# Optimization experiments

Measured on AMD Instinct MI355X. Metric: run time of the kernel, lower is better.

## Reference

```python
import jax, jax.numpy as jnp
import numpy as np

NUM_QUBITS = 512
NUM_CORES = 16
CORE_SIZE = 64
HIDDEN = 128
BATCH = 2048


def setup_inputs() -> dict:
    key = jax.random.key(0)
    k1, k2, k3 = jax.random.split(key, 3)
    last_assignment = jax.random.randint(k1, (BATCH, NUM_QUBITS), 0, NUM_CORES, dtype=jnp.int32)
    adjacency = jnp.ones((NUM_CORES, NUM_CORES), dtype=jnp.float32)  # all-to-all core graph
    qubit_embedding = jax.random.normal(k2, (NUM_QUBITS + 1, HIDDEN), dtype=jnp.float32)
    gcn_weight = jax.random.normal(k3, (HIDDEN, HIDDEN), dtype=jnp.float32) * (1.0 / np.sqrt(HIDDEN))
    gcn_bias = jnp.zeros((HIDDEN,), dtype=jnp.float32)
    return {
        'last_assignment': last_assignment,
        'adjacency': adjacency,
        'qubit_embedding': qubit_embedding,
        'gcn_weight': gcn_weight,
        'gcn_bias': gcn_bias,
    }


def reference(last_assignment, adjacency, qubit_embedding, gcn_weight, gcn_bias):
    B, Q = last_assignment.shape
    C = adjacency.shape[0]
    # --- replace the sequential per-qubit scatter loop with a single cumsum ---
    # pos[b,q] = number of earlier qubits assigned to the same core (the loop's
    # running counter idx); core index C (the extra row) always writes slot 0
    # because the loop resets its counter every iteration.
    oh = jax.nn.one_hot(last_assignment, C + 1, dtype=jnp.int32)        # [B,Q,C+1]
    cnt = jnp.cumsum(oh, axis=1)                                        # inclusive counts
    pos = jnp.take_along_axis(cnt, last_assignment[..., None], axis=2)[..., 0] - 1
    pos = jnp.where(last_assignment == C, 0, pos)
    buf = jnp.full((B, C + 1, CORE_SIZE), Q, dtype=jnp.int32)           # padding id = num_qubits
    b_idx = jnp.arange(B)[:, None]
    q_idx = jnp.broadcast_to(jnp.arange(Q, dtype=jnp.int32)[None, :], (B, Q))
    buf = buf.at[b_idx, last_assignment, pos].set(q_idx, mode='drop')
    buf = buf[:, :C, :]                                                 # drop overflow core row
    # --- embedding (padding row forced to zero, as nn.Embedding padding_idx) ---
    tbl = qubit_embedding.at[Q].set(0.0)
    qubit_embs = tbl[buf]                                               # [B,C,core_size,H]
    core_embs = qubit_embs.max(axis=2)                                  # [B,C,H]
    # --- GCNConv(add_self_loops=False): D^{-1/2} A D^{-1/2} (X W^T) + b ---
    deg = adjacency.sum(axis=0)
    dinv = jnp.where(deg > 0, 1.0 / jnp.sqrt(deg), 0.0)
    a_norm = adjacency * dinv[:, None] * dinv[None, :]                  # symmetric norm
    h = jnp.einsum('bch,oh->bco', core_embs, gcn_weight)                # lin (PyG: x @ W^T)
    out = jnp.einsum('ij,bjo->bio', a_norm, h) + gcn_bias               # [B,C,H]
    return out
```

## Files before the change

kernel.cpp:

```cpp
#include <hip/hip_runtime.h>
#include <stdint.h>

typedef unsigned short u16;
typedef unsigned int u32;
typedef unsigned long long u64;

typedef __bf16 bf16x8 __attribute__((ext_vector_type(8)));
typedef float f32x4 __attribute__((ext_vector_type(4)));
typedef u16 u16x8 __attribute__((ext_vector_type(8)));

#define NQ 512
#define NC 16
#define NH 128
#define NB 2048
#define ESTRIDE 136
#define HSTRIDE 24
#define QE_KEYS (513*128)
#define WT_OFF  QE_KEYS
#define GW_ELEMS (128*128)

static __device__ __forceinline__ u16 f2bf_rne(float f){
  u32 u = __float_as_uint(f);
  u += 0x7fffu + ((u>>16)&1u);
  return (u16)(u>>16);
}
static __device__ __forceinline__ u32 pack_rne(float lo, float hi){
  return (u32)f2bf_rne(lo) | ((u32)f2bf_rne(hi)<<16);
}
static __device__ __forceinline__ u16 key_of(float f){
  u16 b = f2bf_rne(f);
  return (b & 0x8000u) ? (u16)~b : (u16)(b | 0x8000u);
}
static __device__ __forceinline__ u16 unkey(u16 k){
  return (k & 0x8000u) ? (u16)(k ^ 0x8000u) : (u16)~k;
}

union Frag { u32 u[4]; uint4 u4; bf16x8 f; };
union U8   { u16x8 v; int w[4]; uint4 u4; u16 h[8]; };

__global__ void prepass_kernel(const float* __restrict__ qe,
                               const float* __restrict__ gw,
                               u16* __restrict__ ws)
{
  int idx = blockIdx.x * 256 + threadIdx.x;
  if (idx < QE_KEYS/8) {
    int i8 = idx * 8;
    uint4 o;
    if (i8 >= 512*NH) {
      o.x = 0x80008000u; o.y = 0x80008000u; o.z = 0x80008000u; o.w = 0x80008000u;
    } else {
      const float4* p = (const float4*)(qe + i8);
      float4 a = p[0], b = p[1];
      o.x = (u32)key_of(a.x) | ((u32)key_of(a.y)<<16);
      o.y = (u32)key_of(a.z) | ((u32)key_of(a.w)<<16);
      o.z = (u32)key_of(b.x) | ((u32)key_of(b.y)<<16);
      o.w = (u32)key_of(b.z) | ((u32)key_of(b.w)<<16);
    }
    *(uint4*)(ws + i8) = o;
  } else if (idx < QE_KEYS/8 + GW_ELEMS/8) {
    int j8 = (idx - QE_KEYS/8) * 8;
    const float4* p = (const float4*)(gw + j8);
    float4 a = p[0], b = p[1];
    uint4 o;
    o.x = pack_rne(a.x, a.y); o.y = pack_rne(a.z, a.w);
    o.z = pack_rne(b.x, b.y); o.w = pack_rne(b.z, b.w);
    *(uint4*)(ws + WT_OFF + j8) = o;
  }
}

static __device__ __forceinline__ void wave_reduce_max(U8& A){
  U8 B;
  #pragma unroll
  for (int j = 0; j < 4; ++j) B.w[j] = __shfl_xor(A.w[j], 16);
  A.v = __builtin_elementwise_max(A.v, B.v);
  #pragma unroll
  for (int j = 0; j < 4; ++j) B.w[j] = __shfl_xor(A.w[j], 32);
  A.v = __builtin_elementwise_max(A.v, B.v);
}

__global__ __launch_bounds__(256, 4)
void core_snapshot_kernel(const int* __restrict__ la,
                          const float* __restrict__ adj,
                          const u16* __restrict__ ws,
                          const float* __restrict__ gb,
                          float* __restrict__ outp)
{
  __shared__ __align__(16) u16 sE[16*ESTRIDE];
  __shared__ __align__(16) u16 sHB[128*HSTRIDE];
  __shared__ __align__(16) u16 sList[16*64];
  __shared__ u32 sHist[8*16];
  __shared__ u32 sBase[8*16];
  __shared__ u32 sCnt[16];
  __shared__ float sDinv[16];

  const int tid  = threadIdx.x;
  const int lane = tid & 63;
  const int wv   = tid >> 6;
  const int m    = lane & 15;
  const int quad = lane >> 4;
  const int b    = blockIdx.x;
  const u16* qt  = ws;
  const u16* wt  = ws + WT_OFF;

  ((uint2*)sList)[tid] = make_uint2(0x02000200u, 0x02000200u);

  int av[2]; u32 intra[2];
  const u64 lmask = (1ull << lane) - 1ull;
  #pragma unroll
  for (int r = 0; r < 2; ++r) {
    int ch = wv*2 + r;
    av[r] = la[b*NQ + ch*64 + lane];
  }
  #pragma unroll
  for (int r = 0; r < 2; ++r) {
    int ch = wv*2 + r;
    #pragma unroll
    for (int c = 0; c < 16; ++c) {
      u64 mk = __ballot(av[r] == c);
      if (lane == c)  sHist[ch*16 + c] = (u32)__popcll(mk);
      if (av[r] == c) intra[r] = (u32)__popcll(mk & lmask);
    }
  }
  if (tid < 16) {
    float s = 0.f;
    for (int i = 0; i < 16; ++i) s += adj[i*16 + tid];
    sDinv[tid] = (s > 0.f) ? (1.0f / sqrtf(s)) : 0.f;
  }
  __syncthreads();
  if (tid < 16) {
    u32 run = 0;
    #pragma unroll
    for (int ch = 0; ch < 8; ++ch) { sBase[ch*16 + tid] = run; run += sHist[ch*16 + tid]; }
    sCnt[tid] = run;
  }
  __syncthreads();
  #pragma unroll
  for (int r = 0; r < 2; ++r) {
    int ch = wv*2 + r;
    u32 rank = sBase[ch*16 + av[r]] + intra[r];
    if (rank < 64) sList[av[r]*64 + (rank&3)*16 + (rank>>2)] = (u16)(ch*64 + lane);
  }
  __syncthreads();

  {
    const u16* qb = qt + m*8;
    #pragma unroll
    for (int half = 0; half < 2; ++half) {
      const int ca = wv*4 + half*2, cb = ca + 1;
      U8 Sa0, Sa1, Sb0, Sb1;
      Sa0.u4 = *(const uint4*)&sList[ca*64 + quad*16];
      Sa1.u4 = *(const uint4*)&sList[ca*64 + quad*16 + 8];
      Sb0.u4 = *(const uint4*)&sList[cb*64 + quad*16];
      Sb1.u4 = *(const uint4*)&sList[cb*64 + quad*16 + 8];
      const int cna = (int)sCnt[ca], cnb = (int)sCnt[cb];
      U8 A, B; A.v = (u16x8)0; B.v = (u16x8)0;
      {
        U8 Ta[4], Tb[4];
        #pragma unroll
        for (int k = 0; k < 4; ++k) {
          Ta[k].u4 = *(const uint4*)(qb + (int)Sa0.h[k]*NH);
          Tb[k].u4 = *(const uint4*)(qb + (int)Sb0.h[k]*NH);
        }
        #pragma unroll
        for (int k = 0; k < 4; ++k) {
          A.v = __builtin_elementwise_max(A.v, Ta[k].v);
          B.v = __builtin_elementwise_max(B.v, Tb[k].v);
        }
        #pragma unroll
        for (int k = 0; k < 4; ++k) {
          Ta[k].u4 = *(const uint4*)(qb + (int)Sa0.h[k+4]*NH);
          Tb[k].u4 = *(const uint4*)(qb + (int)Sb0.h[k+4]*NH);
        }
        #pragma unroll
        for (int k = 0; k < 4; ++k) {
          A.v = __builtin_elementwise_max(A.v, Ta[k].v);
          B.v = __builtin_elementwise_max(B.v, Tb[k].v);
        }
      }
      if (cna > 32) {
        U8 Ta[8];
        #pragma unroll
        for (int k = 0; k < 8; ++k) Ta[k].u4 = *(const uint4*)(qb + (int)Sa1.h[k]*NH);
        #pragma unroll
        for (int k = 0; k < 8; ++k) A.v = __builtin_elementwise_max(A.v, Ta[k].v);
      }
      if (cnb > 32) {
        U8 Tb[8];
        #pragma unroll
        for (int k = 0; k < 8; ++k) Tb[k].u4 = *(const uint4*)(qb + (int)Sb1.h[k]*NH);
        #pragma unroll
        for (int k = 0; k < 8; ++k) B.v = __builtin_elementwise_max(B.v, Tb[k].v);
      }
      wave_reduce_max(A);
      wave_reduce_max(B);
      U8 Z; Z.v = (u16x8)(u16)0x8000u;
      if (cna < 64) A.v = __builtin_elementwise_max(A.v, Z.v);
      if (cnb < 64) B.v = __builtin_elementwise_max(B.v, Z.v);
      if (quad == 0) {
        uint4 e;
        e.x = (u32)unkey(A.h[0]) | ((u32)unkey(A.h[1])<<16);
        e.y = (u32)unkey(A.h[2]) | ((u32)unkey(A.h[3])<<16);
        e.z = (u32)unkey(A.h[4]) | ((u32)unkey(A.h[5])<<16);
        e.w = (u32)unkey(A.h[6]) | ((u32)unkey(A.h[7])<<16);
        *(uint4*)&sE[ca*ESTRIDE + m*8] = e;
        e.x = (u32)unkey(B.h[0]) | ((u32)unkey(B.h[1])<<16);
        e.y = (u32)unkey(B.h[2]) | ((u32)unkey(B.h[3])<<16);
        e.z = (u32)unkey(B.h[4]) | ((u32)unkey(B.h[5])<<16);
        e.w = (u32)unkey(B.h[6]) | ((u32)unkey(B.h[7])<<16);
        *(uint4*)&sE[cb*ESTRIDE + m*8] = e;
      }
    }
  }
  __syncthreads();

  {
    bf16x8 af[4];
    #pragma unroll
    for (int ks = 0; ks < 4; ++ks)
      af[ks] = *(const bf16x8*)&sE[m*ESTRIDE + ks*32 + quad*8];
    #pragma unroll
    for (int t = 0; t < 2; ++t) {
      int o = (wv*2 + t)*16 + m;
      f32x4 acc = {0.f, 0.f, 0.f, 0.f};
      #pragma unroll
      for (int ks = 0; ks < 4; ++ks) {
        bf16x8 bfr = *(const bf16x8*)(wt + o*NH + ks*32 + quad*8);
        acc = __builtin_amdgcn_mfma_f32_16x16x32_bf16(af[ks], bfr, acc, 0, 0, 0);
      }
      *(u32*)&sHB[o*HSTRIDE + quad*4]     = pack_rne(acc[0], acc[1]);
      *(u32*)&sHB[o*HSTRIDE + quad*4 + 2] = pack_rne(acc[2], acc[3]);
    }
  }
  __syncthreads();

  Frag afr2;
  #pragma unroll
  for (int jj = 0; jj < 4; ++jj) {
    float lo = 0.f, hi = 0.f;
    if (quad < 2) {
      int k0 = quad*8 + jj*2;
      lo = adj[m*16 + k0]     * sDinv[m] * sDinv[k0];
      hi = adj[m*16 + k0 + 1] * sDinv[m] * sDinv[k0 + 1];
    }
    afr2.u[jj] = pack_rne(lo, hi);
  }
  #pragma unroll
  for (int t = 0; t < 2; ++t) {
    int o = (wv*2 + t)*16 + m;
    float biasv = gb[(wv*2 + t)*16 + m];
    Frag bfr;
    if (quad < 2) bfr.u4 = *(const uint4*)&sHB[o*HSTRIDE + quad*8];
    else { bfr.u[0]=0; bfr.u[1]=0; bfr.u[2]=0; bfr.u[3]=0; }
    f32x4 acc = {biasv, biasv, biasv, biasv};
    acc = __builtin_amdgcn_mfma_f32_16x16x32_bf16(afr2.f, bfr.f, acc, 0, 0, 0);
    float* op = outp + b*(NC*NH) + o;
    #pragma unroll
    for (int r = 0; r < 4; ++r) op[(quad*4 + r)*NH] = acc[r];
  }
}

extern "C" void kernel_launch(void* const* d_in, const int* in_sizes, int n_in,
                              void* d_out, int out_size, void* d_ws, size_t ws_size,
                              hipStream_t stream) {
  const int*   la  = (const int*)d_in[0];
  const float* adj = (const float*)d_in[1];
  const float* qe  = (const float*)d_in[2];
  const float* gw  = (const float*)d_in[3];
  const float* gb  = (const float*)d_in[4];
  float* outp = (float*)d_out;
  u16* ws = (u16*)d_ws;

  int pre_threads = QE_KEYS/8 + GW_ELEMS/8;
  prepass_kernel<<<(pre_threads + 255)/256, 256, 0, stream>>>(qe, gw, ws);
  core_snapshot_kernel<<<NB, 256, 0, stream>>>(la, adj, ws, gb, outp);
}
```

Before: 94.70 us.

## Stage embedding table in LDS and process eight batch items per block

The bf16 key table (513x128, about 140KB with padding) is copied into shared memory once per 1024-thread block. Each block then handles 8 batch items, two at a time with two 8-wave teams, so the gathers read LDS instead of global/L2. The launch drops from 2048 blocks to 256. The large LDS footprint allows only one block per CU, and the per-block table load plus the extra barriers in each pair loop could offset the gain.

```diff
diff --git a/kernel.cpp b/kernel.cpp
--- a/kernel.cpp
+++ b/kernel.cpp
@@ -13,8 +13,11 @@
 #define NC 16
 #define NH 128
 #define NB 2048
+#define IPB 8
+#define NBLK (NB/IPB)
+#define TSTRIDE 136
 #define ESTRIDE 136
-#define HSTRIDE 24
+#define HSTRIDE 16
 #define QE_KEYS (513*128)
 #define WT_OFF  QE_KEYS
 #define GW_ELEMS (128*128)
@@ -78,47 +81,41 @@
   A.v = __builtin_elementwise_max(A.v, B.v);
 }
 
-__global__ __launch_bounds__(256, 4)
+__global__ __launch_bounds__(1024, 4)
 void core_snapshot_kernel(const int* __restrict__ la,
                           const float* __restrict__ adj,
                           const u16* __restrict__ ws,
                           const float* __restrict__ gb,
                           float* __restrict__ outp)
 {
-  __shared__ __align__(16) u16 sE[16*ESTRIDE];
-  __shared__ __align__(16) u16 sHB[128*HSTRIDE];
-  __shared__ __align__(16) u16 sList[16*64];
-  __shared__ u32 sHist[8*16];
-  __shared__ u32 sBase[8*16];
-  __shared__ u32 sCnt[16];
+  __shared__ __align__(16) u16 sTab[513*TSTRIDE];
+  __shared__ __align__(16) u16 sList[2][16*64];
+  __shared__ __align__(16) u16 sE[2][16*ESTRIDE];
+  __shared__ __align__(16) u16 sHB[2][128*HSTRIDE];
+  __shared__ u32 sHist[2][8*16];
+  __shared__ u32 sBase[2][8*16];
+  __shared__ u32 sCnt[2][16];
   __shared__ float sDinv[16];
 
   const int tid  = threadIdx.x;
   const int lane = tid & 63;
   const int wv   = tid >> 6;
+  const int team = wv >> 3;
+  const int wt8  = wv & 7;
   const int m    = lane & 15;
   const int quad = lane >> 4;
-  const int b    = blockIdx.x;
-  const u16* qt  = ws;
   const u16* wt  = ws + WT_OFF;
 
-  ((uint2*)sList)[tid] = make_uint2(0x02000200u, 0x02000200u);
-
-  int av[2]; u32 intra[2];
-  const u64 lmask = (1ull << lane) - 1ull;
-  #pragma unroll
-  for (int r = 0; r < 2; ++r) {
-    int ch = wv*2 + r;
-    av[r] = la[b*NQ + ch*64 + lane];
-  }
-  #pragma unroll
-  for (int r = 0; r < 2; ++r) {
-    int ch = wv*2 + r;
+  {
+    const uint4* src = (const uint4*)ws;
     #pragma unroll
-    for (int c = 0; c < 16; ++c) {
-      u64 mk = __ballot(av[r] == c);
-      if (lane == c)  sHist[ch*16 + c] = (u32)__popcll(mk);
-      if (av[r] == c) intra[r] = (u32)__popcll(mk & lmask);
+    for (int i = 0; i < 9; ++i) {
+      int idx = tid + i*1024;
+      if (idx < QE_KEYS/8) {
+        uint4 v = src[idx];
+        int row = idx >> 4, col8 = (idx & 15) << 3;
+        *(uint4*)&sTab[row*TSTRIDE + col8] = v;
+      }
     }
   }
   if (tid < 16) {
@@ -127,39 +124,67 @@
     sDinv[tid] = (s > 0.f) ? (1.0f / sqrtf(s)) : 0.f;
   }
   __syncthreads();
-  if (tid < 16) {
-    u32 run = 0;
+
+  Frag afr2;
+  #pragma unroll
+  for (int jj = 0; jj < 4; ++jj) {
+    float lo = 0.f, hi = 0.f;
+    if (quad < 2) {
+      int k0 = quad*8 + jj*2;
+      lo = adj[m*16 + k0]     * sDinv[m] * sDinv[k0];
+      hi = adj[m*16 + k0 + 1] * sDinv[m] * sDinv[k0 + 1];
+    }
+    afr2.u[jj] = pack_rne(lo, hi);
+  }
+  const int ocol = wt8*16 + m;
+  const float biasv = gb[ocol];
+  const u64 lmask = (1ull << lane) - 1ull;
+
+  for (int pair = 0; pair < IPB/2; ++pair) {
+    const int item = blockIdx.x*IPB + pair*2 + team;
+
+    if (tid < 256)
+      ((uint4*)sList)[tid] = make_uint4(0x02000200u,0x02000200u,0x02000200u,0x02000200u);
+
+    const int avv = la[item*NQ + wt8*64 + lane];
+    u32 intra = 0;
     #pragma unroll
-    for (int ch = 0; ch < 8; ++ch) { sBase[ch*16 + tid] = run; run += sHist[ch*16 + tid]; }
-    sCnt[tid] = run;
-  }
-  __syncthreads();
-  #pragma unroll
-  for (int r = 0; r < 2; ++r) {
-    int ch = wv*2 + r;
-    u32 rank = sBase[ch*16 + av[r]] + intra[r];
-    if (rank < 64) sList[av[r]*64 + (rank&3)*16 + (rank>>2)] = (u16)(ch*64 + lane);
-  }
-  __syncthreads();
-
-  {
-    const u16* qb = qt + m*8;
-    #pragma unroll
-    for (int half = 0; half < 2; ++half) {
-      const int ca = wv*4 + half*2, cb = ca + 1;
+    for (int c = 0; c < 16; ++c) {
+      u64 mk = __ballot(avv == c);
+      if (lane == c) sHist[team][wt8*16 + c] = (u32)__popcll(mk);
+      if (avv == c)  intra = (u32)__popcll(mk & lmask);
+    }
+    __syncthreads();
+    if (tid < 32) {
+      int t = tid >> 4, c = tid & 15;
+      u32 run = 0;
+      #pragma unroll
+      for (int ch = 0; ch < 8; ++ch) { sBase[t][ch*16 + c] = run; run += sHist[t][ch*16 + c]; }
+      sCnt[t][c] = run;
+    }
+    __syncthreads();
+    {
+      u32 rank = sBase[team][wt8*16 + avv] + intra;
+      if (rank < 64) sList[team][avv*64 + (rank&3)*16 + (rank>>2)] = (u16)(wt8*64 + lane);
+    }
+    __syncthreads();
+
+    {
+      const int ca = wt8*2, cb = ca + 1;
       U8 Sa0, Sa1, Sb0, Sb1;
-      Sa0.u4 = *(const uint4*)&sList[ca*64 + quad*16];
-      Sa1.u4 = *(const uint4*)&sList[ca*64 + quad*16 + 8];
-      Sb0.u4 = *(const uint4*)&sList[cb*64 + quad*16];
-      Sb1.u4 = *(const uint4*)&sList[cb*64 + quad*16 + 8];
-      const int cna = (int)sCnt[ca], cnb = (int)sCnt[cb];
+      Sa0.u4 = *(const uint4*)&sList[team][ca*64 + quad*16];
+      Sa1.u4 = *(const uint4*)&sList[team][ca*64 + quad*16 + 8];
+      Sb0.u4 = *(const uint4*)&sList[team][cb*64 + quad*16];
+      Sb1.u4 = *(const uint4*)&sList[team][cb*64 + quad*16 + 8];
+      const int cna = (int)sCnt[team][ca], cnb = (int)sCnt[team][cb];
       U8 A, B; A.v = (u16x8)0; B.v = (u16x8)0;
+      const u16* tb = sTab + m*8;
       {
         U8 Ta[4], Tb[4];
         #pragma unroll
         for (int k = 0; k < 4; ++k) {
-          Ta[k].u4 = *(const uint4*)(qb + (int)Sa0.h[k]*NH);
-          Tb[k].u4 = *(const uint4*)(qb + (int)Sb0.h[k]*NH);
+          Ta[k].u4 = *(const uint4*)(tb + (int)Sa0.h[k]*TSTRIDE);
+          Tb[k].u4 = *(const uint4*)(tb + (int)Sb0.h[k]*TSTRIDE);
         }
         #pragma unroll
         for (int k = 0; k < 4; ++k) {
@@ -168,8 +193,8 @@
         }
         #pragma unroll
         for (int k = 0; k < 4; ++k) {
-          Ta[k].u4 = *(const uint4*)(qb + (int)Sa0.h[k+4]*NH);
-          Tb[k].u4 = *(const uint4*)(qb + (int)Sb0.h[k+4]*NH);
+          Ta[k].u4 = *(const uint4*)(tb + (int)Sa0.h[k+4]*TSTRIDE);
+          Tb[k].u4 = *(const uint4*)(tb + (int)Sb0.h[k+4]*TSTRIDE);
         }
         #pragma unroll
         for (int k = 0; k < 4; ++k) {
@@ -180,14 +205,14 @@
       if (cna > 32) {
         U8 Ta[8];
         #pragma unroll
-        for (int k = 0; k < 8; ++k) Ta[k].u4 = *(const uint4*)(qb + (int)Sa1.h[k]*NH);
+        for (int k = 0; k < 8; ++k) Ta[k].u4 = *(const uint4*)(tb + (int)Sa1.h[k]*TSTRIDE);
         #pragma unroll
         for (int k = 0; k < 8; ++k) A.v = __builtin_elementwise_max(A.v, Ta[k].v);
       }
       if (cnb > 32) {
         U8 Tb[8];
         #pragma unroll
-        for (int k = 0; k < 8; ++k) Tb[k].u4 = *(const uint4*)(qb + (int)Sb1.h[k]*NH);
+        for (int k = 0; k < 8; ++k) Tb[k].u4 = *(const uint4*)(tb + (int)Sb1.h[k]*TSTRIDE);
         #pragma unroll
         for (int k = 0; k < 8; ++k) B.v = __builtin_elementwise_max(B.v, Tb[k].v);
       }
@@ -202,60 +227,43 @@
         e.y = (u32)unkey(A.h[2]) | ((u32)unkey(A.h[3])<<16);
         e.z = (u32)unkey(A.h[4]) | ((u32)unkey(A.h[5])<<16);
         e.w = (u32)unkey(A.h[6]) | ((u32)unkey(A.h[7])<<16);
-        *(uint4*)&sE[ca*ESTRIDE + m*8] = e;
+        *(uint4*)&sE[team][ca*ESTRIDE + m*8] = e;
         e.x = (u32)unkey(B.h[0]) | ((u32)unkey(B.h[1])<<16);
         e.y = (u32)unkey(B.h[2]) | ((u32)unkey(B.h[3])<<16);
         e.z = (u32)unkey(B.h[4]) | ((u32)unkey(B.h[5])<<16);
         e.w = (u32)unkey(B.h[6]) | ((u32)unkey(B.h[7])<<16);
-        *(uint4*)&sE[cb*ESTRIDE + m*8] = e;
-      }
-    }
-  }
-  __syncthreads();
-
-  {
-    bf16x8 af[4];
-    #pragma unroll
-    for (int ks = 0; ks < 4; ++ks)
-      af[ks] = *(const bf16x8*)&sE[m*ESTRIDE + ks*32 + quad*8];
-    #pragma unroll
-    for (int t = 0; t < 2; ++t) {
-      int o = (wv*2 + t)*16 + m;
+        *(uint4*)&sE[team][cb*ESTRIDE + m*8] = e;
+      }
+    }
+    __syncthreads();
+
+    {
+      bf16x8 af[4];
+      #pragma unroll
+      for (int ks = 0; ks < 4; ++ks)
+        af[ks] = *(const bf16x8*)&sE[team][m*ESTRIDE + ks*32 + quad*8];
       f32x4 acc = {0.f, 0.f, 0.f, 0.f};
       #pragma unroll
       for (int ks = 0; ks < 4; ++ks) {
-        bf16x8 bfr = *(const bf16x8*)(wt + o*NH + ks*32 + quad*8);
+        bf16x8 bfr = *(const bf16x8*)(wt + ocol*NH + ks*32 + quad*8);
         acc = __builtin_amdgcn_mfma_f32_16x16x32_bf16(af[ks], bfr, acc, 0, 0, 0);
       }
-      *(u32*)&sHB[o*HSTRIDE + quad*4]     = pack_rne(acc[0], acc[1]);
-      *(u32*)&sHB[o*HSTRIDE + quad*4 + 2] = pack_rne(acc[2], acc[3]);
-    }
-  }
-  __syncthreads();
-
-  Frag afr2;
-  #pragma unroll
-  for (int jj = 0; jj < 4; ++jj) {
-    float lo = 0.f, hi = 0.f;
-    if (quad < 2) {
-      int k0 = quad*8 + jj*2;
-      lo = adj[m*16 + k0]     * sDinv[m] * sDinv[k0];
-      hi = adj[m*16 + k0 + 1] * sDinv[m] * sDinv[k0 + 1];
-    }
-    afr2.u[jj] = pack_rne(lo, hi);
-  }
-  #pragma unroll
-  for (int t = 0; t < 2; ++t) {
-    int o = (wv*2 + t)*16 + m;
-    float biasv = gb[(wv*2 + t)*16 + m];
-    Frag bfr;
-    if (quad < 2) bfr.u4 = *(const uint4*)&sHB[o*HSTRIDE + quad*8];
-    else { bfr.u[0]=0; bfr.u[1]=0; bfr.u[2]=0; bfr.u[3]=0; }
-    f32x4 acc = {biasv, biasv, biasv, biasv};
-    acc = __builtin_amdgcn_mfma_f32_16x16x32_bf16(afr2.f, bfr.f, acc, 0, 0, 0);
-    float* op = outp + b*(NC*NH) + o;
-    #pragma unroll
-    for (int r = 0; r < 4; ++r) op[(quad*4 + r)*NH] = acc[r];
+      *(u32*)&sHB[team][ocol*HSTRIDE + quad*4]     = pack_rne(acc[0], acc[1]);
+      *(u32*)&sHB[team][ocol*HSTRIDE + quad*4 + 2] = pack_rne(acc[2], acc[3]);
+    }
+    __syncthreads();
+
+    {
+      Frag bfr;
+      if (quad < 2) bfr.u4 = *(const uint4*)&sHB[team][ocol*HSTRIDE + quad*8];
+      else { bfr.u[0]=0; bfr.u[1]=0; bfr.u[2]=0; bfr.u[3]=0; }
+      f32x4 acc = {biasv, biasv, biasv, biasv};
+      acc = __builtin_amdgcn_mfma_f32_16x16x32_bf16(afr2.f, bfr.f, acc, 0, 0, 0);
+      float* op = outp + item*(NC*NH) + ocol;
+      #pragma unroll
+      for (int r = 0; r < 4; ++r) op[(quad*4 + r)*NH] = acc[r];
+    }
+    __syncthreads();
   }
 }
 
@@ -272,5 +280,5 @@
 
   int pre_threads = QE_KEYS/8 + GW_ELEMS/8;
   prepass_kernel<<<(pre_threads + 255)/256, 256, 0, stream>>>(qe, gw, ws);
-  core_snapshot_kernel<<<NB, 256, 0, stream>>>(la, adj, ws, gb, outp);
-}
+  core_snapshot_kernel<<<NBLK, 1024, 0, stream>>>(la, adj, ws, gb, outp);
+}
```

Result: no change. 95.92 us (+1.3%).
